# Kernel optimization log

Hardware: AMD Instinct MI355X
Metric: run time of the kernel (lower is better)

## Reference

```python
import jax, jax.numpy as jnp
import numpy as np

B, N, D, H = 64, 197, 768, 12
HD = D // H          # 64
MLP = 4 * D          # 3072
WIN = 14
NUM_REL = (2 * WIN - 1) * (2 * WIN - 1) + 3  # 732
SCALE = HD ** -0.5
DCF_SCALE = 1.0
EPS = 1e-5


def _make_rel_index(wh, ww):
    coords = np.stack(np.meshgrid(np.arange(wh), np.arange(ww), indexing='ij'))  # [2, wh, ww]
    flat = coords.reshape(2, -1)
    rel = flat[:, :, None] - flat[:, None, :]          # [2, L, L]
    rel = rel.transpose(1, 2, 0).astype(np.int64)      # [L, L, 2]
    rel[..., 0] += wh - 1
    rel[..., 1] += ww - 1
    rel[..., 0] *= 2 * ww - 1
    idx = np.zeros((wh * ww + 1, wh * ww + 1), dtype=np.int32)
    idx[1:, 1:] = rel.sum(-1)
    nrd = (2 * wh - 1) * (2 * ww - 1) + 3
    idx[0, :] = nrd - 3
    idx[:, 0] = nrd - 2
    idx[0, 0] = nrd - 1
    return idx


def _ln(x, w, b):
    m = x.mean(-1, keepdims=True)
    v = ((x - m) ** 2).mean(-1, keepdims=True)
    return (x - m) * jax.lax.rsqrt(v + EPS) * w + b


def setup_inputs() -> dict:
    key = jax.random.key(0)
    ks = jax.random.split(key, 32)
    rnd = lambda i, shp, s=0.02: jax.random.normal(ks[i], shp, jnp.float32) * s
    return {
        'x': jax.random.normal(ks[0], (B, N, D), jnp.float32),
        'w_qkv': rnd(1, (3 * D, D)),
        'q_bias': rnd(2, (D,)),
        'v_bias': rnd(3, (D,)),
        'ssf_scale_qkv': 1.0 + rnd(4, (3 * D,)),
        'ssf_shift_qkv': rnd(5, (3 * D,)),
        'rel_bias_table': rnd(6, (NUM_REL, H)),
        'bases_coeff': rnd(7, (H, H)),
        'w_proj': rnd(8, (D, D)),
        'b_proj': rnd(9, (D,)),
        'ssf_scale_proj': 1.0 + rnd(10, (D,)),
        'ssf_shift_proj': rnd(11, (D,)),
        'norm1_w': jnp.ones((D,), jnp.float32),
        'norm1_b': jnp.zeros((D,), jnp.float32),
        'norm2_w': jnp.ones((D,), jnp.float32),
        'norm2_b': jnp.zeros((D,), jnp.float32),
        'ssf_scale_1': 1.0 + rnd(12, (D,)),
        'ssf_shift_1': rnd(13, (D,)),
        'ssf_scale_2': 1.0 + rnd(14, (D,)),
        'ssf_shift_2': rnd(15, (D,)),
        'w_fc1': rnd(16, (MLP, D)),
        'b_fc1': rnd(17, (MLP,)),
        'w_fc2': rnd(18, (D, MLP)),
        'b_fc2': rnd(19, (D,)),
        'ssf_scale_mlp': 1.0 + rnd(20, (D,)),
        'ssf_shift_mlp': rnd(21, (D,)),
        'gamma_1': jnp.full((D,), 0.1, jnp.float32),
        'gamma_2': jnp.full((D,), 0.1, jnp.float32),
        'rel_pos_index': jnp.asarray(_make_rel_index(WIN, WIN)),
    }


def reference(x, w_qkv, q_bias, v_bias, ssf_scale_qkv, ssf_shift_qkv,
              rel_bias_table, bases_coeff, w_proj, b_proj,
              ssf_scale_proj, ssf_shift_proj, norm1_w, norm1_b, norm2_w, norm2_b,
              ssf_scale_1, ssf_shift_1, ssf_scale_2, ssf_shift_2,
              w_fc1, b_fc1, w_fc2, b_fc2, ssf_scale_mlp, ssf_shift_mlp,
              gamma_1, gamma_2, rel_pos_index):
    # --- attention branch (eval mode: all dropouts are identity) ---
    h = _ln(x, norm1_w, norm1_b) * ssf_scale_1 + ssf_shift_1
    qkv_bias = jnp.concatenate([q_bias, jnp.zeros_like(v_bias), v_bias])
    qkv = h @ w_qkv.T + qkv_bias                       # [B, N, 3D]
    qkv = qkv * ssf_scale_qkv + ssf_shift_qkv
    qkv = qkv.reshape(B, N, 3, H, HD).transpose(2, 0, 3, 1, 4)  # [3, B, H, N, hd]
    q, k, v = qkv[0] * SCALE, qkv[1], qkv[2]
    attn = jnp.einsum('bhnd,bhmd->bhnm', q, k)         # [B, H, N, N]
    bias = rel_bias_table[rel_pos_index.reshape(-1)].reshape(N, N, H).transpose(2, 0, 1)
    attn = jax.nn.softmax(attn + bias[None], axis=-1)
    # dcf head mixing
    coeff = bases_coeff.T * DCF_SCALE + jnp.eye(H, dtype=attn.dtype)
    attn = jnp.einsum('bhnl,hk->bknl', attn, coeff)
    y = jnp.einsum('bhnm,bhmd->bnhd', attn, v).reshape(B, N, D)
    y = y @ w_proj.T + b_proj
    y = y * ssf_scale_proj + ssf_shift_proj
    x = x + gamma_1 * y
    # --- MLP branch ---
    h = _ln(x, norm2_w, norm2_b) * ssf_scale_2 + ssf_shift_2
    m = jax.nn.gelu(h @ w_fc1.T + b_fc1, approximate=False)
    m = m @ w_fc2.T + b_fc2
    m = m * ssf_scale_mlp + ssf_shift_mlp
    return x + gamma_2 * m
```

## Files before the change

kernel.cpp:

```cpp
#include <hip/hip_runtime.h>

typedef unsigned short u16;
using f32x4  = __attribute__((ext_vector_type(4))) float;
using bf16x8 = __attribute__((ext_vector_type(8))) __bf16;

#define Bz   64
#define Nn   197
#define Dd   768
#define Hh   12
#define HDp  64
#define MLPD 3072
#define ROWS (Bz*Nn)
#define NM   (Nn*Nn)
#define NPAD 224

#define OFF_H    0UL
#define OFF_X1   19365888UL
#define OFF_BIA  58097664UL
#define OFF_WB   59960496UL
#define OFF_CH   74116272UL
#define WQKV_E 0UL
#define WPRJ_E 1769472UL
#define WFC1_E 2359296UL
#define WFC2_E 4718592UL
#define QKV_B  907776UL
#define P_B    1059072UL
#define VT_B   344064UL
#define CHUNK_B 2310912UL

__device__ inline float b2f(u16 v){ unsigned u = ((unsigned)v) << 16; float f; __builtin_memcpy(&f,&u,4); return f; }
__device__ inline u16 f2b(float f){ unsigned u; __builtin_memcpy(&u,&f,4); u += 0x7FFFu + ((u>>16)&1u); return (u16)(u>>16); }

__device__ inline float gelu_f(float x){
    float z  = fabsf(x) * 0.70710678118f;
    float t  = 1.f / (1.f + 0.3275911f * z);
    float y  = t*(0.254829592f + t*(-0.284496736f + t*(1.421413741f + t*(-1.453152027f + t*1.061405429f))));
    float er = 1.f - y * __expf(-z*z);
    er = copysignf(er, x);
    return 0.5f * x * (1.f + er);
}

__device__ inline void gload_lds16(const u16* g, u16* l) {
    __builtin_amdgcn_global_load_lds((const __attribute__((address_space(1))) void*)g,
                                     (__attribute__((address_space(3))) void*)l, 16, 0, 0);
}

__global__ __launch_bounds__(256)
void conv_b16(const float* __restrict__ src, u16* __restrict__ dst, int n4)
{
    int t = blockIdx.x*256 + threadIdx.x;
    if (t >= n4) return;
    float4 v = *(const float4*)(src + (size_t)t*4);
    u16* d = dst + (size_t)t*4;
    d[0] = f2b(v.x); d[1] = f2b(v.y); d[2] = f2b(v.z); d[3] = f2b(v.w);
}

template<int EPI>
__global__ __launch_bounds__(256, 2)
void gemm128p(const u16* __restrict__ A, const u16* __restrict__ W, void* __restrict__ Cp,
              int M, int N, int K, int lda, int ldw,
              const float* __restrict__ e0, const float* __restrict__ e1,
              const float* __restrict__ e2, const float* __restrict__ e3,
              const float* __restrict__ e4, const float* __restrict__ ef)
{
    extern __shared__ u16 lds[];
    constexpr int SWEEP = 2048;
    constexpr int ICA  = 2;
    constexpr int ICB  = 2;
    constexpr int ASZ  = 128 * 32;
    constexpr int BSZ  = 128 * 32;
    constexpr int ABUF = 2 * ASZ;
    constexpr int BBUF = 2 * BSZ;
    constexpr int MF   = 4;
    constexpr int MH   = 2;

    u16* sA = lds;
    u16* sB = lds + 2 * ABUF;

    const int tid  = threadIdx.x;
    const int lane = tid & 63;
    const int wave = tid >> 6;
    const int wr   = wave >> 1;
    const int wc   = wave & 1;
    const int rid  = lane & 15;
    const int kg   = lane >> 4;
    const int m0   = blockIdx.y * 128;
    const int n0   = blockIdx.x * 128;
    const int t8   = tid * 8;

    const u16* asrc[2][ICA]; int adst[2][ICA];
    const u16* bsrc[2][ICB]; int bdst[2][ICB];
#pragma unroll
    for (int s = 0; s < 2; ++s) {
#pragma unroll
        for (int i = 0; i < ICA; ++i) {
            int e = i*SWEEP + t8, r = e >> 5;
            int g = ((e >> 3) & 3) ^ ((r >> 1) & 3);
            int row = m0 + r; if (row > M-1) row = M-1;
            asrc[s][i] = A + (size_t)row*lda + s*32 + g*8;
            adst[s][i] = s*ASZ + e;
        }
#pragma unroll
        for (int i = 0; i < ICB; ++i) {
            int e = i*SWEEP + t8, r = e >> 5;
            int g = ((e >> 3) & 3) ^ ((r >> 1) & 3);
            int col = n0 + r; if (col > N-1) col = N-1;
            bsrc[s][i] = W + (size_t)col*ldw + s*32 + g*8;
            bdst[s][i] = s*BSZ + e;
        }
    }

    const int koA   = (kg ^ ((rid >> 1) & 3)) * 8;
    const int aRow0 = (wr*64 + rid) * 32 + koA;
    const int bRow  = (wc*64 + rid) * 32 + koA;

    f32x4 acc[MF][4];
#pragma unroll
    for (int i = 0; i < MF; ++i)
#pragma unroll
        for (int j = 0; j < 4; ++j) acc[i][j] = (f32x4){0.f,0.f,0.f,0.f};

#define WAITBAR() asm volatile("s_waitcnt vmcnt(4) lgkmcnt(0)\n\ts_barrier" ::: "memory")

#pragma unroll
    for (int i = 0; i < ICA; ++i) gload_lds16(asrc[0][i], sA + adst[0][i]);
#pragma unroll
    for (int i = 0; i < ICB; ++i) gload_lds16(bsrc[0][i], sB + bdst[0][i]);
    asm volatile("" ::: "memory");
#pragma unroll
    for (int i = 0; i < ICA; ++i) gload_lds16(asrc[1][i], sA + adst[1][i]);
#pragma unroll
    for (int i = 0; i < ICB; ++i) gload_lds16(bsrc[1][i], sB + bdst[1][i]);
    WAITBAR();

    const int NT = K >> 6;
    for (int t = 0; t < NT; ++t) {
        const int p  = t & 1;
        const size_t kpre = (size_t)(t + 1) * 64;
        const u16* paB = sA + p * ABUF;
        const u16* pbB = sB + p * BBUF;
        const int  qa  = (p ^ 1) * ABUF;
        const int  qb  = (p ^ 1) * BBUF;
        bf16x8 af[MH], wf[4];

        {
            const u16* pa = paB + aRow0;
#pragma unroll
            for (int f = 0; f < MH; ++f) af[f] = *(const bf16x8*)(pa + f*512);
            const u16* pb = pbB + bRow;
#pragma unroll
            for (int j = 0; j < 4; ++j) wf[j] = *(const bf16x8*)(pb + j*512);
#pragma unroll
            for (int i = 0; i < ICA; ++i) gload_lds16(asrc[0][i] + kpre, sA + adst[0][i] + qa);
            __builtin_amdgcn_s_setprio(1);
#pragma unroll
            for (int f = 0; f < MH; ++f)
#pragma unroll
                for (int j = 0; j < 4; ++j)
                    acc[f][j] = __builtin_amdgcn_mfma_f32_16x16x32_bf16(af[f], wf[j], acc[f][j], 0, 0, 0);
            __builtin_amdgcn_s_setprio(0);
        }
        {
            const u16* pa = paB + aRow0 + MH*512;
#pragma unroll
            for (int f = 0; f < MH; ++f) af[f] = *(const bf16x8*)(pa + f*512);
#pragma unroll
            for (int i = 0; i < ICB; ++i) gload_lds16(bsrc[0][i] + kpre, sB + bdst[0][i] + qb);
            __builtin_amdgcn_s_setprio(1);
#pragma unroll
            for (int f = 0; f < MH; ++f)
#pragma unroll
                for (int j = 0; j < 4; ++j)
                    acc[MH+f][j] = __builtin_amdgcn_mfma_f32_16x16x32_bf16(af[f], wf[j], acc[MH+f][j], 0, 0, 0);
            __builtin_amdgcn_s_setprio(0);
        }
        WAITBAR();
        {
            const u16* pa = paB + ASZ + aRow0;
#pragma unroll
            for (int f = 0; f < MH; ++f) af[f] = *(const bf16x8*)(pa + f*512);
            const u16* pb = pbB + BSZ + bRow;
#pragma unroll
            for (int j = 0; j < 4; ++j) wf[j] = *(const bf16x8*)(pb + j*512);
#pragma unroll
            for (int i = 0; i < ICA; ++i) gload_lds16(asrc[1][i] + kpre, sA + adst[1][i] + qa);
            __builtin_amdgcn_s_setprio(1);
#pragma unroll
            for (int f = 0; f < MH; ++f)
#pragma unroll
                for (int j = 0; j < 4; ++j)
                    acc[f][j] = __builtin_amdgcn_mfma_f32_16x16x32_bf16(af[f], wf[j], acc[f][j], 0, 0, 0);
            __builtin_amdgcn_s_setprio(0);
        }
        {
            const u16* pa = paB + ASZ + aRow0 + MH*512;
#pragma unroll
            for (int f = 0; f < MH; ++f) af[f] = *(const bf16x8*)(pa + f*512);
#pragma unroll
            for (int i = 0; i < ICB; ++i) gload_lds16(bsrc[1][i] + kpre, sB + bdst[1][i] + qb);
            __builtin_amdgcn_s_setprio(1);
#pragma unroll
            for (int f = 0; f < MH; ++f)
#pragma unroll
                for (int j = 0; j < 4; ++j)
                    acc[MH+f][j] = __builtin_amdgcn_mfma_f32_16x16x32_bf16(af[f], wf[j], acc[MH+f][j], 0, 0, 0);
            __builtin_amdgcn_s_setprio(0);
        }
        WAITBAR();
    }
    asm volatile("s_waitcnt vmcnt(0)" ::: "memory");
    __syncthreads();
#undef WAITBAR

    float* ka = (float*)(lds + 2*ABUF);
    float* kb = ka + 128;
    if (tid < 128) {
        int gn = n0 + tid;
        if constexpr (EPI == 0) {
            float mql = (gn < 768) ? 0.125f : 1.f;
            float bias = 0.f;
            if (gn < 768) bias = e0[gn];
            else if (gn >= 1536) bias = e1[gn-1536];
            float sc = e2[gn];
            ka[tid] = sc * mql;
            kb[tid] = (bias * sc + e3[gn]) * mql;
        } else if constexpr (EPI == 4) {
            ka[tid] = 0.f;
            kb[tid] = e0[gn];
        } else {
            float sc = e1[gn];
            ka[tid] = sc;
            kb[tid] = e0[gn]*sc + e2[gn];
        }
    }
    __syncthreads();

    const int rq = (lane >> 4) * 4;
    const int cc = lane & 15;
    float kaj[4], kbj[4];
#pragma unroll
    for (int j = 0; j < 4; ++j) {
        int c = wc*64 + j*16 + cc;
        kaj[j] = ka[c]; kbj[j] = kb[c];
    }

    if constexpr (EPI == 0 || EPI == 4) {
        u16* ct = lds;
#pragma unroll
        for (int i = 0; i < MF; ++i) {
#pragma unroll
            for (int j = 0; j < 4; ++j) {
#pragma unroll
                for (int r = 0; r < 4; ++r) {
                    int rowL = wr*64 + i*16 + rq + r;
                    int col  = wc*64 + j*16 + cc;
                    float v = acc[i][j][r];
                    u16 o;
                    if constexpr (EPI == 0) o = f2b(v*kaj[j] + kbj[j]);
                    else                    o = f2b(gelu_f(v + kbj[j]));
                    ct[rowL*128 + col] = o;
                }
            }
        }
        __syncthreads();
        constexpr int ldc = (EPI == 0) ? 2304 : 3072;
        u16* C = (u16*)Cp;
#pragma unroll
        for (int sw = 0; sw < 8; ++sw) {
            int rowL = sw*16 + (tid >> 4);
            int gm = m0 + rowL;
            if (gm < M) {
                int col0 = (tid & 15) * 8;
                *(uint4*)(C + (size_t)gm*ldc + n0 + col0) =
                    *(const uint4*)(ct + rowL*128 + col0);
            }
        }
    } else {
        float* cf = (float*)lds;
        const float* RES = (EPI == 3) ? e4 : ef;
        float* C = (float*)Cp;
#pragma unroll
        for (int h = 0; h < 2; ++h) {
            if (wr == h) {
#pragma unroll
                for (int i = 0; i < MF; ++i) {
#pragma unroll
                    for (int j = 0; j < 4; ++j) {
#pragma unroll
                        for (int r = 0; r < 4; ++r) {
                            int rowH = i*16 + rq + r;
                            int col  = wc*64 + j*16 + cc;
                            cf[rowH*128 + col] = acc[i][j][r]*kaj[j] + kbj[j];
                        }
                    }
                }
            }
            __syncthreads();
#pragma unroll
            for (int sw = 0; sw < 8; ++sw) {
                int rowH = sw*8 + (tid >> 5);
                int gm = m0 + h*64 + rowH;
                if (gm < M) {
                    int col0 = (tid & 31) * 4;
                    f32x4 v  = *(const f32x4*)(cf + rowH*128 + col0);
                    size_t gidx = (size_t)gm*768 + n0 + col0;
                    f32x4 xv = *(const f32x4*)(RES + gidx);
                    f32x4 g3 = *(const f32x4*)(e3 + n0 + col0);
                    f32x4 o;
#pragma unroll
                    for (int q = 0; q < 4; ++q) o[q] = xv[q] + g3[q]*v[q];
                    *(f32x4*)(C + gidx) = o;
                }
            }
            __syncthreads();
        }
    }
}

template<int EPI>
__global__ __launch_bounds__(256)
void gemm_nt(const u16* __restrict__ A, const u16* __restrict__ W, void* __restrict__ Cp,
             int M, int N, int K, int lda, int ldw, int b0,
             const float* __restrict__ ef)
{
    __shared__ __align__(16) u16 csm[(EPI == 1) ? 32768 : 16384];
    const int tid  = threadIdx.x;
    const int lane = tid & 63;
    const int wave = tid >> 6;
    const int z    = blockIdx.z;
    const int m0   = wave*64;
    const int n0   = blockIdx.x*64;
    const int rid  = lane & 15;
    const int kq   = (lane >> 4) * 8;

    const u16* Ab = A;
    const u16* Wb = W;
    if constexpr (EPI == 1) {
        int bb = z/12, hh = z - bb*12;
        Ab = A + ((size_t)bb*Nn)*2304 + hh*64;
        Wb = W + ((size_t)bb*Nn)*2304 + 768 + hh*64;
    } else {
        Ab = A + (size_t)z*Nn*NPAD;
        Wb = W + (size_t)z*HDp*NPAD;
    }

    f32x4 acc[4][4];
#pragma unroll
    for (int i = 0; i < 4; ++i)
#pragma unroll
        for (int j = 0; j < 4; ++j) acc[i][j] = (f32x4){0.f,0.f,0.f,0.f};

    for (int k0 = 0; k0 < K; k0 += 32) {
        bf16x8 af[4], wf[4];
#pragma unroll
        for (int i = 0; i < 4; ++i) {
            int r = m0 + i*16 + rid; if (r > M-1) r = M-1;
            af[i] = *(const bf16x8*)(Ab + (size_t)r*lda + k0 + kq);
        }
#pragma unroll
        for (int j = 0; j < 4; ++j) {
            int c = n0 + j*16 + rid; if (c > N-1) c = N-1;
            wf[j] = *(const bf16x8*)(Wb + (size_t)c*ldw + k0 + kq);
        }
#pragma unroll
        for (int i = 0; i < 4; ++i)
#pragma unroll
            for (int j = 0; j < 4; ++j)
                acc[i][j] = __builtin_amdgcn_mfma_f32_16x16x32_bf16(af[i], wf[j], acc[i][j], 0, 0, 0);
    }

    const int rq = (lane >> 4) * 4;
    const int cc = lane & 15;

    if constexpr (EPI == 1) {
        float* cs = (float*)csm;
#pragma unroll
        for (int i = 0; i < 4; ++i)
#pragma unroll
            for (int j = 0; j < 4; ++j)
#pragma unroll
                for (int r = 0; r < 4; ++r)
                    cs[(m0 + i*16 + rq + r)*64 + j*16 + cc] = acc[i][j][r];
        __syncthreads();
        int hh = z - (z/12)*12;
        const float* bsrc = ef + (size_t)hh*NM;
        u16* P = (u16*)Cp + (size_t)z*Nn*NPAD;
        for (int sw = 0; sw < 13; ++sw) {
            int row = sw*16 + (tid >> 4);
            int col0 = (tid & 15) * 4;
            int gn = n0 + col0;
            if (row < Nn && gn < NPAD) {
                f32x4 v = *(const f32x4*)(cs + row*64 + col0);
                const float* bp = bsrc + (size_t)row*Nn + gn;
                float b0v = bp[0], b1v = bp[1], b2v = bp[2], b3v = bp[3];
                unsigned lo = (unsigned)f2b(v[0]+b0v) | ((unsigned)f2b(v[1]+b1v) << 16);
                unsigned hi = (unsigned)f2b(v[2]+b2v) | ((unsigned)f2b(v[3]+b3v) << 16);
                uint2 pk; pk.x = lo; pk.y = hi;
                *(uint2*)(P + (size_t)row*NPAD + gn) = pk;
            }
        }
    } else {
        u16* cs = csm;
#pragma unroll
        for (int i = 0; i < 4; ++i)
#pragma unroll
            for (int j = 0; j < 4; ++j)
#pragma unroll
                for (int r = 0; r < 4; ++r)
                    cs[(m0 + i*16 + rq + r)*64 + j*16 + cc] = f2b(acc[i][j][r]);
        __syncthreads();
        int bb = z/12, kk = z - bb*12;
        u16* Y = (u16*)Cp + ((size_t)(b0+bb)*Nn)*768 + kk*64;
        for (int sw = 0; sw < 7; ++sw) {
            int row = sw*32 + (tid >> 3);
            if (row < Nn) {
                int col0 = (tid & 7) * 8;
                *(uint4*)(Y + (size_t)row*768 + col0) = *(const uint4*)(cs + row*64 + col0);
            }
        }
    }
}

__global__ __launch_bounds__(256)
void ln_ssf(const float* __restrict__ x, const float* __restrict__ w, const float* __restrict__ bb,
            const float* __restrict__ sc, const float* __restrict__ sh, u16* __restrict__ out)
{
    const int row = blockIdx.x, tid = threadIdx.x;
    const float* xr = x + (size_t)row * 768;
    float v[3], s1 = 0.f, s2 = 0.f;
#pragma unroll
    for (int i = 0; i < 3; ++i) {
        float f = xr[tid + i*256];
        v[i] = f; s1 += f; s2 += f*f;
    }
    for (int o = 32; o > 0; o >>= 1) { s1 += __shfl_xor(s1, o); s2 += __shfl_xor(s2, o); }
    __shared__ float r1[4], r2[4];
    int wv = tid >> 6;
    if ((tid & 63) == 0) { r1[wv] = s1; r2[wv] = s2; }
    __syncthreads();
    s1 = r1[0]+r1[1]+r1[2]+r1[3];
    s2 = r2[0]+r2[1]+r2[2]+r2[3];
    float mean = s1 * (1.f/768.f);
    float var  = s2 * (1.f/768.f) - mean*mean;
    float rstd = rsqrtf(fmaxf(var, 0.f) + 1e-5f);
#pragma unroll
    for (int i = 0; i < 3; ++i) {
        int c = tid + i*256;
        float h = (v[i] - mean) * rstd * w[c] + bb[c];
        h = h * sc[c] + sh[c];
        out[(size_t)row*768 + c] = f2b(h);
    }
}

__global__ __launch_bounds__(256)
void bias_gather(const int* __restrict__ idx, const float* __restrict__ table, float* __restrict__ biasf)
{
    int t = blockIdx.x*256 + threadIdx.x;
    if (t >= NM) return;
    int id = idx[t];
#pragma unroll
    for (int h = 0; h < 12; ++h)
        biasf[(size_t)h*NM + t] = table[id*12 + h];
}

__global__ __launch_bounds__(256)
void softmax_dcf(u16* __restrict__ P, const float* __restrict__ bases, int nb)
{
    __shared__ float cf[144];
    int tid = threadIdx.x;
    if (tid < 144) {
        int k = tid / 12, h = tid - k*12;
        cf[h*12 + k] = bases[k*12 + h] + (h == k ? 1.f : 0.f);
    }
    __syncthreads();
    int ridx = blockIdx.x*4 + (tid >> 6);
    if (ridx >= nb*Nn) return;
    int lane = tid & 63;
    int m0 = lane * 4;
    int bb = ridx / Nn, n = ridx - bb*Nn;
    const size_t hs = (size_t)Nn*NPAD;
    u16* base = P + ((size_t)bb*12)*hs + (size_t)n*NPAD;

    float e[12][4];
#pragma unroll
    for (int h = 0; h < 12; ++h) {
        float s[4];
        if (m0 < NPAD) {
            uint2 pv = *(const uint2*)(base + h*hs + m0);
            s[0] = b2f((u16)(pv.x & 0xFFFF)); s[1] = b2f((u16)(pv.x >> 16));
            s[2] = b2f((u16)(pv.y & 0xFFFF)); s[3] = b2f((u16)(pv.y >> 16));
        } else { s[0]=s[1]=s[2]=s[3] = -1e30f; }
#pragma unroll
        for (int j = 0; j < 4; ++j) if (m0 + j >= Nn) s[j] = -1e30f;
        float mx = fmaxf(fmaxf(s[0], s[1]), fmaxf(s[2], s[3]));
        for (int o = 32; o > 0; o >>= 1) mx = fmaxf(mx, __shfl_xor(mx, o));
        float sum = 0.f;
#pragma unroll
        for (int j = 0; j < 4; ++j) {
            float ev = __expf(fmaxf(s[j] - mx, -80.f));
            if (m0 + j >= Nn) ev = 0.f;
            e[h][j] = ev; sum += ev;
        }
        for (int o = 32; o > 0; o >>= 1) sum += __shfl_xor(sum, o);
        float inv = 1.f / sum;
#pragma unroll
        for (int j = 0; j < 4; ++j) e[h][j] *= inv;
    }
    if (m0 < NPAD) {
#pragma unroll
        for (int k = 0; k < 12; ++k) {
            float o0 = 0.f, o1 = 0.f, o2 = 0.f, o3 = 0.f;
#pragma unroll
            for (int h = 0; h < 12; ++h) {
                float c = cf[h*12 + k];
                o0 += e[h][0]*c; o1 += e[h][1]*c; o2 += e[h][2]*c; o3 += e[h][3]*c;
            }
            unsigned lo = (unsigned)f2b(o0) | ((unsigned)f2b(o1) << 16);
            unsigned hi = (unsigned)f2b(o2) | ((unsigned)f2b(o3) << 16);
            uint2 pk; pk.x = lo; pk.y = hi;
            *(uint2*)(base + k*hs + m0) = pk;
        }
    }
}

__global__ __launch_bounds__(256)
void v_transpose(const u16* __restrict__ qkv, u16* __restrict__ vT)
{
    __shared__ u16 lds[64*198];
    int z = blockIdx.x;
    int bb = z/12, hh = z - bb*12;
    int tid = threadIdx.x;
    const u16* src = qkv + ((size_t)bb*Nn)*2304 + 1536 + hh*64;
    for (int e = tid; e < Nn*64; e += 256) {
        int m = e >> 6, d = e & 63;
        lds[d*198 + m] = src[(size_t)m*2304 + d];
    }
    __syncthreads();
    u16* dst = vT + (size_t)z*64*NPAD;
    for (int e = tid; e < 64*NPAD; e += 256) {
        int d = e / NPAD, m = e - d*NPAD;
        dst[e] = (m < Nn) ? lds[d*198 + m] : (u16)0;
    }
}

extern "C" void kernel_launch(void* const* d_in, const int* in_sizes, int n_in,
                              void* d_out, int out_size, void* d_ws, size_t ws_size,
                              hipStream_t stream)
{
    const float* x       = (const float*)d_in[0];
    const float* w_qkv   = (const float*)d_in[1];
    const float* q_bias  = (const float*)d_in[2];
    const float* v_bias  = (const float*)d_in[3];
    const float* s_qkv   = (const float*)d_in[4];
    const float* sh_qkv  = (const float*)d_in[5];
    const float* rel_tab = (const float*)d_in[6];
    const float* bases   = (const float*)d_in[7];
    const float* w_proj  = (const float*)d_in[8];
    const float* b_proj  = (const float*)d_in[9];
    const float* s_proj  = (const float*)d_in[10];
    const float* sh_proj = (const float*)d_in[11];
    const float* n1w     = (const float*)d_in[12];
    const float* n1b     = (const float*)d_in[13];
    const float* n2w     = (const float*)d_in[14];
    const float* n2b     = (const float*)d_in[15];
    const float* ss1     = (const float*)d_in[16];
    const float* ssh1    = (const float*)d_in[17];
    const float* ss2     = (const float*)d_in[18];
    const float* ssh2    = (const float*)d_in[19];
    const float* w_fc1   = (const float*)d_in[20];
    const float* b_fc1   = (const float*)d_in[21];
    const float* w_fc2   = (const float*)d_in[22];
    const float* b_fc2   = (const float*)d_in[23];
    const float* s_mlp   = (const float*)d_in[24];
    const float* sh_mlp  = (const float*)d_in[25];
    const float* g1      = (const float*)d_in[26];
    const float* g2      = (const float*)d_in[27];
    const int*   relidx  = (const int*)d_in[28];

    char*  ws   = (char*)d_ws;
    u16*   hbuf = (u16*)(ws + OFF_H);
    float* x1   = (float*)(ws + OFF_X1);
    float* bia  = (float*)(ws + OFF_BIA);
    u16*   wb   = (u16*)(ws + OFF_WB);
    float* out  = (float*)d_out;

    u16* wqkvB = wb + WQKV_E;
    u16* wprjB = wb + WPRJ_E;
    u16* wfc1B = wb + WFC1_E;
    u16* wfc2B = wb + WFC2_E;

    hipFuncSetAttribute(reinterpret_cast<const void*>(&gemm128p<0>),
                        hipFuncAttributeMaxDynamicSharedMemorySize, 65536);
    hipFuncSetAttribute(reinterpret_cast<const void*>(&gemm128p<3>),
                        hipFuncAttributeMaxDynamicSharedMemorySize, 65536);
    hipFuncSetAttribute(reinterpret_cast<const void*>(&gemm128p<4>),
                        hipFuncAttributeMaxDynamicSharedMemorySize, 65536);
    hipFuncSetAttribute(reinterpret_cast<const void*>(&gemm128p<5>),
                        hipFuncAttributeMaxDynamicSharedMemorySize, 65536);

    int nb = 64;
    while (nb > 1 && OFF_CH + (size_t)nb*CHUNK_B > ws_size) nb >>= 1;
    const int nchunk = 64 / nb;
    u16* qkvC = (u16*)(ws + OFF_CH);
    u16* PC   = (u16*)(ws + OFF_CH + (size_t)nb*QKV_B);
    u16* vTC  = (u16*)(ws + OFF_CH + (size_t)nb*(QKV_B + P_B));

    conv_b16<<<dim3(1728), dim3(256), 0, stream>>>(w_qkv, wqkvB, 442368);
    conv_b16<<<dim3(576),  dim3(256), 0, stream>>>(w_proj, wprjB, 147456);
    conv_b16<<<dim3(2304), dim3(256), 0, stream>>>(w_fc1, wfc1B, 589824);
    conv_b16<<<dim3(2304), dim3(256), 0, stream>>>(w_fc2, wfc2B, 589824);

    ln_ssf<<<dim3(ROWS), dim3(256), 0, stream>>>(x, n1w, n1b, ss1, ssh1, hbuf);
    bias_gather<<<dim3(152), dim3(256), 0, stream>>>(relidx, rel_tab, bia);

    for (int c = 0; c < nchunk; ++c) {
        const int b0 = c * nb;
        const int nrows = nb * Nn;
        const int gy = (nrows + 127) / 128;
        gemm128p<0><<<dim3(18, gy), dim3(256), 65536, stream>>>(
            hbuf + (size_t)b0*Nn*768, wqkvB, qkvC,
            nrows, 2304, 768, 768, 768, q_bias, v_bias, s_qkv, sh_qkv, nullptr, nullptr);
        v_transpose<<<dim3(nb*12), dim3(256), 0, stream>>>(qkvC, vTC);
        gemm_nt<1><<<dim3(4, 1, nb*12), dim3(256), 0, stream>>>(
            qkvC, qkvC, PC, Nn, Nn, 64, 2304, 2304, 0, bia);
        softmax_dcf<<<dim3((nb*Nn + 3)/4), dim3(256), 0, stream>>>(PC, bases, nb);
        gemm_nt<2><<<dim3(1, 1, nb*12), dim3(256), 0, stream>>>(
            PC, vTC, hbuf, Nn, 64, NPAD, NPAD, NPAD, b0, nullptr);
    }

    gemm128p<3><<<dim3(6, 99), dim3(256), 65536, stream>>>(
        hbuf, wprjB, x1, ROWS, 768, 768, 768, 768,
        b_proj, s_proj, sh_proj, g1, x, nullptr);
    ln_ssf<<<dim3(ROWS), dim3(256), 0, stream>>>(x1, n2w, n2b, ss2, ssh2, hbuf);

    u16* mlpC = qkvC;
    size_t avail = (ws_size > OFF_CH) ? (ws_size - OFF_CH) : (size_t)CHUNK_B;
    int nrM = (int)(avail / (MLPD * 2));
    if (nrM < 1) nrM = 1;
    if (nrM > ROWS) nrM = ROWS;
    for (int r0 = 0; r0 < ROWS; r0 += nrM) {
        int cr = ROWS - r0; if (cr > nrM) cr = nrM;
        int gy = (cr + 127) / 128;
        gemm128p<4><<<dim3(24, gy), dim3(256), 65536, stream>>>(
            hbuf + (size_t)r0*768, wfc1B, mlpC, cr, 3072, 768, 768, 768,
            b_fc1, nullptr, nullptr, nullptr, nullptr, nullptr);
        gemm128p<5><<<dim3(6, gy), dim3(256), 65536, stream>>>(
            mlpC, wfc2B, out + (size_t)r0*768, cr, 768, 3072, 3072, 3072,
            b_fc2, s_mlp, sh_mlp, g2, nullptr, x1 + (size_t)r0*768);
    }
}
```

Before: 707.2 us.

## Add 256x256-tile 512-thread GEMM for QKV, FC1 and FC2 projections

Adds a gemm256v kernel that uses 256x256 output tiles, 8 waves and 128KB of LDS, and routes the QKV, FC1 and FC2 GEMMs through it. gemm128p is kept only for the output projection, so its epilogue is cut down to that one case. The larger tile raises arithmetic intensity and cuts global/L2 traffic per FLOP. In exchange there are far fewer blocks (e.g. 3x50 for FC2), which hurts occupancy and load balance across the CUs, and the last M tile wastes more work.

```diff
diff --git a/kernel.cpp b/kernel.cpp
--- a/kernel.cpp
+++ b/kernel.cpp
@@ -53,6 +53,267 @@
     float4 v = *(const float4*)(src + (size_t)t*4);
     u16* d = dst + (size_t)t*4;
     d[0] = f2b(v.x); d[1] = f2b(v.y); d[2] = f2b(v.z); d[3] = f2b(v.w);
+}
+
+template<int EPI>
+__global__ __launch_bounds__(512, 1)
+void gemm256v(const u16* __restrict__ A, const u16* __restrict__ W, void* __restrict__ Cp,
+              int M, int N, int K, int lda, int ldw,
+              const float* __restrict__ e0, const float* __restrict__ e1,
+              const float* __restrict__ e2, const float* __restrict__ e3,
+              const float* __restrict__ ef)
+{
+    extern __shared__ u16 lds[];
+    constexpr int SWEEP = 4096;
+    constexpr int ICA  = 2;
+    constexpr int ICB  = 2;
+    constexpr int ASZ  = 256 * 32;
+    constexpr int BSZ  = 256 * 32;
+    constexpr int ABUF = 2 * ASZ;
+    constexpr int BBUF = 2 * BSZ;
+    constexpr int MF   = 8;
+    constexpr int MH   = 4;
+
+    u16* sA = lds;
+    u16* sB = lds + 2 * ABUF;
+
+    const int tid  = threadIdx.x;
+    const int lane = tid & 63;
+    const int wave = tid >> 6;
+    const int wr   = wave >> 2;
+    const int wc   = wave & 3;
+    const int rid  = lane & 15;
+    const int kg   = lane >> 4;
+    const int m0   = blockIdx.y * 256;
+    const int n0   = blockIdx.x * 256;
+    const int t8   = tid * 8;
+
+    const u16* asrc[2][ICA]; int adst[2][ICA];
+    const u16* bsrc[2][ICB]; int bdst[2][ICB];
+#pragma unroll
+    for (int s = 0; s < 2; ++s) {
+#pragma unroll
+        for (int i = 0; i < ICA; ++i) {
+            int e = i*SWEEP + t8, r = e >> 5;
+            int g = ((e >> 3) & 3) ^ ((r >> 1) & 3);
+            int row = m0 + r; if (row > M-1) row = M-1;
+            asrc[s][i] = A + (size_t)row*lda + s*32 + g*8;
+            adst[s][i] = s*ASZ + e;
+        }
+#pragma unroll
+        for (int i = 0; i < ICB; ++i) {
+            int e = i*SWEEP + t8, r = e >> 5;
+            int g = ((e >> 3) & 3) ^ ((r >> 1) & 3);
+            int col = n0 + r; if (col > N-1) col = N-1;
+            bsrc[s][i] = W + (size_t)col*ldw + s*32 + g*8;
+            bdst[s][i] = s*BSZ + e;
+        }
+    }
+
+    const int koA   = (kg ^ ((rid >> 1) & 3)) * 8;
+    const int aRow0 = (wr*128 + rid) * 32 + koA;
+    const int bRow  = (wc*64  + rid) * 32 + koA;
+
+    f32x4 acc[MF][4];
+#pragma unroll
+    for (int i = 0; i < MF; ++i)
+#pragma unroll
+        for (int j = 0; j < 4; ++j) acc[i][j] = (f32x4){0.f,0.f,0.f,0.f};
+
+#define WAITBAR() asm volatile("s_waitcnt vmcnt(4) lgkmcnt(0)\n\ts_barrier" ::: "memory")
+
+#pragma unroll
+    for (int i = 0; i < ICA; ++i) gload_lds16(asrc[0][i], sA + adst[0][i]);
+#pragma unroll
+    for (int i = 0; i < ICB; ++i) gload_lds16(bsrc[0][i], sB + bdst[0][i]);
+    asm volatile("" ::: "memory");
+#pragma unroll
+    for (int i = 0; i < ICA; ++i) gload_lds16(asrc[1][i], sA + adst[1][i]);
+#pragma unroll
+    for (int i = 0; i < ICB; ++i) gload_lds16(bsrc[1][i], sB + bdst[1][i]);
+    WAITBAR();
+
+    const int NT = K >> 6;
+    for (int t = 0; t < NT; ++t) {
+        const int p  = t & 1;
+        const size_t kpre = (size_t)(t + 1) * 64;
+        const u16* paB = sA + p * ABUF;
+        const u16* pbB = sB + p * BBUF;
+        const int  qa  = (p ^ 1) * ABUF;
+        const int  qb  = (p ^ 1) * BBUF;
+        bf16x8 af[MH], wf[4];
+
+        {
+            const u16* pa = paB + aRow0;
+#pragma unroll
+            for (int f = 0; f < MH; ++f) af[f] = *(const bf16x8*)(pa + f*512);
+            const u16* pb = pbB + bRow;
+#pragma unroll
+            for (int j = 0; j < 4; ++j) wf[j] = *(const bf16x8*)(pb + j*512);
+#pragma unroll
+            for (int i = 0; i < ICA; ++i) gload_lds16(asrc[0][i] + kpre, sA + adst[0][i] + qa);
+            __builtin_amdgcn_s_setprio(1);
+#pragma unroll
+            for (int f = 0; f < MH; ++f)
+#pragma unroll
+                for (int j = 0; j < 4; ++j)
+                    acc[f][j] = __builtin_amdgcn_mfma_f32_16x16x32_bf16(af[f], wf[j], acc[f][j], 0, 0, 0);
+            __builtin_amdgcn_s_setprio(0);
+        }
+        {
+            const u16* pa = paB + aRow0 + MH*512;
+#pragma unroll
+            for (int f = 0; f < MH; ++f) af[f] = *(const bf16x8*)(pa + f*512);
+#pragma unroll
+            for (int i = 0; i < ICB; ++i) gload_lds16(bsrc[0][i] + kpre, sB + bdst[0][i] + qb);
+            __builtin_amdgcn_s_setprio(1);
+#pragma unroll
+            for (int f = 0; f < MH; ++f)
+#pragma unroll
+                for (int j = 0; j < 4; ++j)
+                    acc[MH+f][j] = __builtin_amdgcn_mfma_f32_16x16x32_bf16(af[f], wf[j], acc[MH+f][j], 0, 0, 0);
+            __builtin_amdgcn_s_setprio(0);
+        }
+        WAITBAR();
+        {
+            const u16* pa = paB + ASZ + aRow0;
+#pragma unroll
+            for (int f = 0; f < MH; ++f) af[f] = *(const bf16x8*)(pa + f*512);
+            const u16* pb = pbB + BSZ + bRow;
+#pragma unroll
+            for (int j = 0; j < 4; ++j) wf[j] = *(const bf16x8*)(pb + j*512);
+#pragma unroll
+            for (int i = 0; i < ICA; ++i) gload_lds16(asrc[1][i] + kpre, sA + adst[1][i] + qa);
+            __builtin_amdgcn_s_setprio(1);
+#pragma unroll
+            for (int f = 0; f < MH; ++f)
+#pragma unroll
+                for (int j = 0; j < 4; ++j)
+                    acc[f][j] = __builtin_amdgcn_mfma_f32_16x16x32_bf16(af[f], wf[j], acc[f][j], 0, 0, 0);
+            __builtin_amdgcn_s_setprio(0);
+        }
+        {
+            const u16* pa = paB + ASZ + aRow0 + MH*512;
+#pragma unroll
+            for (int f = 0; f < MH; ++f) af[f] = *(const bf16x8*)(pa + f*512);
+#pragma unroll
+            for (int i = 0; i < ICB; ++i) gload_lds16(bsrc[1][i] + kpre, sB + bdst[1][i] + qb);
+            __builtin_amdgcn_s_setprio(1);
+#pragma unroll
+            for (int f = 0; f < MH; ++f)
+#pragma unroll
+                for (int j = 0; j < 4; ++j)
+                    acc[MH+f][j] = __builtin_amdgcn_mfma_f32_16x16x32_bf16(af[f], wf[j], acc[MH+f][j], 0, 0, 0);
+            __builtin_amdgcn_s_setprio(0);
+        }
+        WAITBAR();
+    }
+    asm volatile("s_waitcnt vmcnt(0)" ::: "memory");
+    __syncthreads();
+#undef WAITBAR
+
+    float* ka = (float*)lds;
+    float* kb = ka + 256;
+    if (tid < 256) {
+        int gn = n0 + tid;
+        if constexpr (EPI == 0) {
+            float mql = (gn < 768) ? 0.125f : 1.f;
+            float bias = 0.f;
+            if (gn < 768) bias = e0[gn];
+            else if (gn >= 1536) bias = e1[gn-1536];
+            float sc = e2[gn];
+            ka[tid] = sc * mql;
+            kb[tid] = (bias * sc + e3[gn]) * mql;
+        } else if constexpr (EPI == 4) {
+            ka[tid] = 0.f;
+            kb[tid] = e0[gn];
+        } else {
+            float sc = e1[gn];
+            ka[tid] = sc;
+            kb[tid] = e0[gn]*sc + e2[gn];
+        }
+    }
+    __syncthreads();
+    const int rq = (lane >> 4) * 4;
+    const int cc = lane & 15;
+    float kaj[4], kbj[4];
+#pragma unroll
+    for (int j = 0; j < 4; ++j) {
+        int c = wc*64 + j*16 + cc;
+        kaj[j] = ka[c]; kbj[j] = kb[c];
+    }
+    __syncthreads();
+
+    if constexpr (EPI == 0 || EPI == 4) {
+        u16* ct = lds;
+#pragma unroll
+        for (int i = 0; i < MF; ++i) {
+#pragma unroll
+            for (int j = 0; j < 4; ++j) {
+#pragma unroll
+                for (int r = 0; r < 4; ++r) {
+                    int rowL = wr*128 + i*16 + rq + r;
+                    int col  = wc*64 + j*16 + cc;
+                    float v = acc[i][j][r];
+                    u16 o;
+                    if constexpr (EPI == 0) o = f2b(v*kaj[j] + kbj[j]);
+                    else                    o = f2b(gelu_f(v + kbj[j]));
+                    ct[rowL*256 + col] = o;
+                }
+            }
+        }
+        __syncthreads();
+        constexpr int ldc = (EPI == 0) ? 2304 : 3072;
+        u16* C = (u16*)Cp;
+#pragma unroll
+        for (int sw = 0; sw < 16; ++sw) {
+            int rowL = sw*16 + (tid >> 5);
+            int gm = m0 + rowL;
+            if (gm < M) {
+                int col0 = (tid & 31) * 8;
+                *(uint4*)(C + (size_t)gm*ldc + n0 + col0) =
+                    *(const uint4*)(ct + rowL*256 + col0);
+            }
+        }
+    } else {
+        float* cf = (float*)lds;
+        float* C = (float*)Cp;
+#pragma unroll
+        for (int h = 0; h < 2; ++h) {
+            if (wr == h) {
+#pragma unroll
+                for (int i = 0; i < MF; ++i) {
+#pragma unroll
+                    for (int j = 0; j < 4; ++j) {
+#pragma unroll
+                        for (int r = 0; r < 4; ++r) {
+                            int rowH = i*16 + rq + r;
+                            int col  = wc*64 + j*16 + cc;
+                            cf[rowH*256 + col] = acc[i][j][r]*kaj[j] + kbj[j];
+                        }
+                    }
+                }
+            }
+            __syncthreads();
+#pragma unroll
+            for (int sw = 0; sw < 16; ++sw) {
+                int rowH = sw*8 + (tid >> 6);
+                int gm = m0 + h*128 + rowH;
+                if (gm < M) {
+                    int col0 = (tid & 63) * 4;
+                    f32x4 v  = *(const f32x4*)(cf + rowH*256 + col0);
+                    size_t gidx = (size_t)gm*768 + n0 + col0;
+                    f32x4 xv = *(const f32x4*)(ef + gidx);
+                    f32x4 g3 = *(const f32x4*)(e3 + n0 + col0);
+                    f32x4 o;
+#pragma unroll
+                    for (int q = 0; q < 4; ++q) o[q] = xv[q] + g3[q]*v[q];
+                    *(f32x4*)(C + gidx) = o;
+                }
+            }
+            __syncthreads();
+        }
+    }
 }
 
 template<int EPI>
@@ -216,22 +477,9 @@
     float* kb = ka + 128;
     if (tid < 128) {
         int gn = n0 + tid;
-        if constexpr (EPI == 0) {
-            float mql = (gn < 768) ? 0.125f : 1.f;
-            float bias = 0.f;
-            if (gn < 768) bias = e0[gn];
-            else if (gn >= 1536) bias = e1[gn-1536];
-            float sc = e2[gn];
-            ka[tid] = sc * mql;
-            kb[tid] = (bias * sc + e3[gn]) * mql;
-        } else if constexpr (EPI == 4) {
-            ka[tid] = 0.f;
-            kb[tid] = e0[gn];
-        } else {
-            float sc = e1[gn];
-            ka[tid] = sc;
-            kb[tid] = e0[gn]*sc + e2[gn];
-        }
+        float sc = e1[gn];
+        ka[tid] = sc;
+        kb[tid] = e0[gn]*sc + e2[gn];
     }
     __syncthreads();
 
@@ -244,76 +492,43 @@
         kaj[j] = ka[c]; kbj[j] = kb[c];
     }
 
-    if constexpr (EPI == 0 || EPI == 4) {
-        u16* ct = lds;
-#pragma unroll
-        for (int i = 0; i < MF; ++i) {
-#pragma unroll
-            for (int j = 0; j < 4; ++j) {
-#pragma unroll
-                for (int r = 0; r < 4; ++r) {
-                    int rowL = wr*64 + i*16 + rq + r;
-                    int col  = wc*64 + j*16 + cc;
-                    float v = acc[i][j][r];
-                    u16 o;
-                    if constexpr (EPI == 0) o = f2b(v*kaj[j] + kbj[j]);
-                    else                    o = f2b(gelu_f(v + kbj[j]));
-                    ct[rowL*128 + col] = o;
-                }
-            }
-        }
-        __syncthreads();
-        constexpr int ldc = (EPI == 0) ? 2304 : 3072;
-        u16* C = (u16*)Cp;
-#pragma unroll
-        for (int sw = 0; sw < 8; ++sw) {
-            int rowL = sw*16 + (tid >> 4);
-            int gm = m0 + rowL;
-            if (gm < M) {
-                int col0 = (tid & 15) * 8;
-                *(uint4*)(C + (size_t)gm*ldc + n0 + col0) =
-                    *(const uint4*)(ct + rowL*128 + col0);
-            }
-        }
-    } else {
-        float* cf = (float*)lds;
-        const float* RES = (EPI == 3) ? e4 : ef;
-        float* C = (float*)Cp;
-#pragma unroll
-        for (int h = 0; h < 2; ++h) {
-            if (wr == h) {
-#pragma unroll
-                for (int i = 0; i < MF; ++i) {
-#pragma unroll
-                    for (int j = 0; j < 4; ++j) {
-#pragma unroll
-                        for (int r = 0; r < 4; ++r) {
-                            int rowH = i*16 + rq + r;
-                            int col  = wc*64 + j*16 + cc;
-                            cf[rowH*128 + col] = acc[i][j][r]*kaj[j] + kbj[j];
-                        }
+    float* cf = (float*)lds;
+    const float* RES = e4;
+    float* C = (float*)Cp;
+#pragma unroll
+    for (int h = 0; h < 2; ++h) {
+        if (wr == h) {
+#pragma unroll
+            for (int i = 0; i < MF; ++i) {
+#pragma unroll
+                for (int j = 0; j < 4; ++j) {
+#pragma unroll
+                    for (int r = 0; r < 4; ++r) {
+                        int rowH = i*16 + rq + r;
+                        int col  = wc*64 + j*16 + cc;
+                        cf[rowH*128 + col] = acc[i][j][r]*kaj[j] + kbj[j];
                     }
                 }
             }
-            __syncthreads();
-#pragma unroll
-            for (int sw = 0; sw < 8; ++sw) {
-                int rowH = sw*8 + (tid >> 5);
-                int gm = m0 + h*64 + rowH;
-                if (gm < M) {
-                    int col0 = (tid & 31) * 4;
-                    f32x4 v  = *(const f32x4*)(cf + rowH*128 + col0);
-                    size_t gidx = (size_t)gm*768 + n0 + col0;
-                    f32x4 xv = *(const f32x4*)(RES + gidx);
-                    f32x4 g3 = *(const f32x4*)(e3 + n0 + col0);
-                    f32x4 o;
-#pragma unroll
-                    for (int q = 0; q < 4; ++q) o[q] = xv[q] + g3[q]*v[q];
-                    *(f32x4*)(C + gidx) = o;
-                }
+        }
+        __syncthreads();
+#pragma unroll
+        for (int sw = 0; sw < 8; ++sw) {
+            int rowH = sw*8 + (tid >> 5);
+            int gm = m0 + h*64 + rowH;
+            if (gm < M) {
+                int col0 = (tid & 31) * 4;
+                f32x4 v  = *(const f32x4*)(cf + rowH*128 + col0);
+                size_t gidx = (size_t)gm*768 + n0 + col0;
+                f32x4 xv = *(const f32x4*)(RES + gidx);
+                f32x4 g3 = *(const f32x4*)(e3 + n0 + col0);
+                f32x4 o;
+#pragma unroll
+                for (int q = 0; q < 4; ++q) o[q] = xv[q] + g3[q]*v[q];
+                *(f32x4*)(C + gidx) = o;
             }
-            __syncthreads();
-        }
+        }
+        __syncthreads();
     }
 }
 
@@ -589,13 +804,13 @@
     u16* wfc1B = wb + WFC1_E;
     u16* wfc2B = wb + WFC2_E;
 
-    hipFuncSetAttribute(reinterpret_cast<const void*>(&gemm128p<0>),
-                        hipFuncAttributeMaxDynamicSharedMemorySize, 65536);
+    hipFuncSetAttribute(reinterpret_cast<const void*>(&gemm256v<0>),
+                        hipFuncAttributeMaxDynamicSharedMemorySize, 131072);
+    hipFuncSetAttribute(reinterpret_cast<const void*>(&gemm256v<4>),
+                        hipFuncAttributeMaxDynamicSharedMemorySize, 131072);
+    hipFuncSetAttribute(reinterpret_cast<const void*>(&gemm256v<5>),
+                        hipFuncAttributeMaxDynamicSharedMemorySize, 131072);
     hipFuncSetAttribute(reinterpret_cast<const void*>(&gemm128p<3>),
-                        hipFuncAttributeMaxDynamicSharedMemorySize, 65536);
-    hipFuncSetAttribute(reinterpret_cast<const void*>(&gemm128p<4>),
-                        hipFuncAttributeMaxDynamicSharedMemorySize, 65536);
-    hipFuncSetAttribute(reinterpret_cast<const void*>(&gemm128p<5>),
                         hipFuncAttributeMaxDynamicSharedMemorySize, 65536);
 
     int nb = 64;
@@ -616,10 +831,10 @@
     for (int c = 0; c < nchunk; ++c) {
         const int b0 = c * nb;
         const int nrows = nb * Nn;
-        const int gy = (nrows + 127) / 128;
-        gemm128p<0><<<dim3(18, gy), dim3(256), 65536, stream>>>(
+        const int gy = (nrows + 255) / 256;
+        gemm256v<0><<<dim3(9, gy), dim3(512), 131072, stream>>>(
             hbuf + (size_t)b0*Nn*768, wqkvB, qkvC,
-            nrows, 2304, 768, 768, 768, q_bias, v_bias, s_qkv, sh_qkv, nullptr, nullptr);
+            nrows, 2304, 768, 768, 768, q_bias, v_bias, s_qkv, sh_qkv, nullptr);
         v_transpose<<<dim3(nb*12), dim3(256), 0, stream>>>(qkvC, vTC);
         gemm_nt<1><<<dim3(4, 1, nb*12), dim3(256), 0, stream>>>(
             qkvC, qkvC, PC, Nn, Nn, 64, 2304, 2304, 0, bia);
@@ -640,12 +855,12 @@
     if (nrM > ROWS) nrM = ROWS;
     for (int r0 = 0; r0 < ROWS; r0 += nrM) {
         int cr = ROWS - r0; if (cr > nrM) cr = nrM;
-        int gy = (cr + 127) / 128;
-        gemm128p<4><<<dim3(24, gy), dim3(256), 65536, stream>>>(
+        int gy = (cr + 255) / 256;
+        gemm256v<4><<<dim3(12, gy), dim3(512), 131072, stream>>>(
             hbuf + (size_t)r0*768, wfc1B, mlpC, cr, 3072, 768, 768, 768,
-            b_fc1, nullptr, nullptr, nullptr, nullptr, nullptr);
-        gemm128p<5><<<dim3(6, gy), dim3(256), 65536, stream>>>(
+            b_fc1, nullptr, nullptr, nullptr, nullptr);
+        gemm256v<5><<<dim3(3, gy), dim3(512), 131072, stream>>>(
             mlpC, wfc2B, out + (size_t)r0*768, cr, 768, 3072, 3072, 3072,
-            b_fc2, s_mlp, sh_mlp, g2, nullptr, x1 + (size_t)r0*768);
-    }
-}
+            b_fc2, s_mlp, sh_mlp, g2, x1 + (size_t)r0*768);
+    }
+}
```

After: 672.5 us. -4.9%, faster.
